# Optimization experiments

Measured on AMD Instinct MI355X. Metric: run time of the kernel, lower is better.

The kernel has to match this reference:

```python
import jax, jax.numpy as jnp
import numpy as np

N = 30000      # nodes
E = 1000000    # edges
G = 256        # graphs
IN = 3         # in_channels
H = 8          # heads
D = 16         # per-head dim
HID = 128      # hidden_dim = H*D
L = 3          # num_layers
KP = 17        # num_keypoints
KPE = 16       # kp_emb_dim
NEG = 0.2      # GATv2 leaky_relu negative slope
EPS = 1e-5     # BatchNorm eps


def setup_inputs() -> dict:
    key = jax.random.key(0)
    ks = jax.random.split(key, 24)
    x = jax.random.normal(ks[0], (N, IN), jnp.float32)
    edge_index = jax.random.randint(ks[1], (2, E), 0, N, jnp.int32)
    batch = jnp.sort(jax.random.randint(ks[2], (N,), 0, G, jnp.int32))
    s_in = 1.0 / np.sqrt(IN + KPE)
    s_h = 1.0 / np.sqrt(HID)
    return {
        "x": x,
        "edge_index": edge_index,
        "batch": batch,
        "kp_emb": jax.random.normal(ks[3], (KP, KPE), jnp.float32),
        "w_in": jax.random.normal(ks[4], (IN + KPE, HID), jnp.float32) * s_in,
        "b_in": jax.random.normal(ks[5], (HID,), jnp.float32) * 0.01,
        "w_l": jax.random.normal(ks[6], (L, HID, HID), jnp.float32) * s_h,
        "w_r": jax.random.normal(ks[7], (L, HID, HID), jnp.float32) * s_h,
        "att": jax.random.normal(ks[8], (L, H, D), jnp.float32) * (1.0 / np.sqrt(D)),
        "conv_bias": jax.random.normal(ks[9], (L, HID), jnp.float32) * 0.01,
        "bn_gamma": jnp.ones((L, HID), jnp.float32) + 0.1 * jax.random.normal(ks[10], (L, HID), jnp.float32),
        "bn_beta": 0.1 * jax.random.normal(ks[11], (L, HID), jnp.float32),
        "bn_mean": 0.1 * jax.random.normal(ks[12], (L, HID), jnp.float32),
        "bn_var": 0.5 + jax.random.uniform(ks[13], (L, HID), jnp.float32),
        "w1": jax.random.normal(ks[14], (HID, 2 * HID), jnp.float32) * s_h,
        "b1": jnp.zeros((2 * HID,), jnp.float32),
        "w2": jax.random.normal(ks[15], (2 * HID, HID), jnp.float32) * (1.0 / np.sqrt(2 * HID)),
        "b2": jnp.zeros((HID,), jnp.float32),
        "w3": jax.random.normal(ks[16], (HID, 2), jnp.float32) * s_h,
        "b3": jnp.zeros((2,), jnp.float32),
    }


def reference(x, edge_index, batch, kp_emb, w_in, b_in, w_l, w_r, att, conv_bias,
              bn_gamma, bn_beta, bn_mean, bn_var, w1, b1, w2, b2, w3, b3):
    n = x.shape[0]
    # keypoint id embedding concat + input projection
    kp_ids = jnp.arange(n) % KP
    h = jnp.concatenate([x, kp_emb[kp_ids]], axis=-1) @ w_in + b_in  # [N, HID]
    # GATv2Conv adds self loops by default
    loops = jnp.arange(n, dtype=edge_index.dtype)
    src = jnp.concatenate([edge_index[0], loops])  # message sources (j)
    dst = jnp.concatenate([edge_index[1], loops])  # message targets (i)
    for l in range(L):
        xl = (h @ w_l[l]).reshape(n, H, D)  # source transform (lin_l)
        xr = (h @ w_r[l]).reshape(n, H, D)  # target transform (lin_r)
        z = xl[src] + xr[dst]                              # [Et, H, D]
        score = jnp.einsum('ehd,hd->eh', jax.nn.leaky_relu(z, NEG), att[l])
        # segment softmax over incoming edges of each dst node
        m = jax.ops.segment_max(score, dst, num_segments=n)
        ex = jnp.exp(score - m[dst])
        denom = jax.ops.segment_sum(ex, dst, num_segments=n)
        alpha = ex / denom[dst]                            # [Et, H]
        msg = xl[src] * alpha[..., None]                   # [Et, H, D]
        out = jax.ops.segment_sum(msg, dst, num_segments=n).reshape(n, HID) + conv_bias[l]
        out = jax.nn.relu(out)
        # BatchNorm1d (eval mode: running stats)
        out = (out - bn_mean[l]) * (bn_gamma[l] / jnp.sqrt(bn_var[l] + EPS)) + bn_beta[l]
        h = h + out  # residual (dropout = identity in eval)
    # global mean pool per graph
    sums = jax.ops.segment_sum(h, batch, num_segments=G)
    cnt = jax.ops.segment_sum(jnp.ones((n, 1), h.dtype), batch, num_segments=G)
    g = sums / jnp.maximum(cnt, 1.0)
    # classifier MLP
    g = jax.nn.elu(g @ w1 + b1)
    g = jax.nn.elu(g @ w2 + b2)
    return g @ w3 + b3  # [G, 2]
```

## Files before the change

### kernel.cpp

```cpp
#include <hip/hip_runtime.h>
#include <hip/hip_bf16.h>

#define N_NODES 30000
#define N_EDGES 1000000
#define N_GRAPHS 256
#define HEADS 8
#define DHEAD 16
#define HIDDEN 128
#define LAYERS 3
#define KPN 17
#define KPE 16
#define NEG_SLOPE 0.2f
#define BN_EPS 1e-5f
#define ET (N_EDGES + N_NODES)
#define NBIN 235
#define BINW 128
#define BINCAP 6144
#define CHUNK 4096
#define NB_EDGE 245
#define NBGEMM 938

typedef __attribute__((ext_vector_type(8))) short bf16x8;
typedef __attribute__((ext_vector_type(4))) float f32x4;

__device__ __forceinline__ unsigned bf16_rne(float f) {
    unsigned u = __float_as_uint(f);
    return (u + 0x7fffu + ((u >> 16) & 1u)) >> 16;
}

__global__ __launch_bounds__(256) void k_pre(const int* __restrict__ batch,
                                             int* __restrict__ bcnt,
                                             int* __restrict__ gptr,
                                             int* __restrict__ ptr,
                                             const float* __restrict__ w_l,
                                             const float* __restrict__ w_r,
                                             unsigned short* __restrict__ wT) {
    int bid = blockIdx.x, t = threadIdx.x;
    if (bid == 0) {
        if (t < NBIN) bcnt[t] = 0;
        for (int g = t; g <= N_GRAPHS; g += 256) {
            if (g == N_GRAPHS) { gptr[g] = N_NODES; }
            else {
                int lo = 0, hi = N_NODES;
                while (lo < hi) {
                    int mid = (lo + hi) >> 1;
                    if (batch[mid] < g) lo = mid + 1; else hi = mid;
                }
                gptr[g] = lo;
            }
        }
        if (t == 0) ptr[N_NODES] = ET;
    } else {
        int idx = (bid - 1) * 256 + t;
        if (idx < LAYERS * 256 * 128) {
            int l = idx / (256 * 128);
            int rem = idx - l * 256 * 128;
            int c = rem >> 7;
            int k = rem & 127;
            float v = (c < 128) ? w_l[(size_t)l * 16384 + k * 128 + c]
                                : w_r[(size_t)l * 16384 + k * 128 + (c - 128)];
            wT[idx] = (unsigned short)bf16_rne(v);
        }
    }
}

template<bool FUSED>
__global__ __launch_bounds__(256) void k_gemmT(const float* __restrict__ x,
                                               const float* __restrict__ kp_emb,
                                               const float* __restrict__ w_in,
                                               const float* __restrict__ b_in,
                                               float* __restrict__ h,
                                               const unsigned short* __restrict__ hb,
                                               const unsigned short* __restrict__ wT,
                                               unsigned short* __restrict__ xlb,
                                               unsigned short* __restrict__ xrb,
                                               const int* __restrict__ ei,
                                               int* __restrict__ bcnt,
                                               unsigned* __restrict__ bdata) {
    __shared__ unsigned short hsA[32][136];
    __shared__ unsigned short st[32][264];
    __shared__ int lcnt[NBIN];
    __shared__ int lbase[NBIN];
    int tid = threadIdx.x;

    if (FUSED && blockIdx.x >= NBGEMM) {
        int base = (blockIdx.x - NBGEMM) * CHUNK;
        int n = N_EDGES - base; if (n > CHUNK) n = CHUNK;
        for (int i = tid; i < NBIN; i += 256) lcnt[i] = 0;
        __syncthreads();
        for (int t = tid; t < n; t += 256) {
            int d = ei[N_EDGES + base + t];
            atomicAdd(&lcnt[d >> 7], 1);
        }
        __syncthreads();
        for (int i = tid; i < NBIN; i += 256) {
            int c = lcnt[i];
            lbase[i] = c ? atomicAdd(&bcnt[i], c) : 0;
            lcnt[i] = 0;
        }
        __syncthreads();
        for (int t = tid; t < n; t += 256) {
            int s = ei[base + t];
            int d = ei[N_EDGES + base + t];
            int b = d >> 7;
            int pos = lbase[b] + atomicAdd(&lcnt[b], 1);
            bdata[(size_t)b * BINCAP + pos] = (unsigned)s | ((unsigned)(d & 127) << 15);
        }
        return;
    }

    int wave = tid >> 6, lane = tid & 63;
    int brow = blockIdx.x * 32;
    int lr = lane & 15, lk = lane >> 4;

    if (FUSED) {
        int r = tid >> 3, c16 = (tid & 7) * 16;
        int gr = brow + r;
        int gc = gr < N_NODES ? gr : 0;
        float xv0 = x[gc * 3], xv1 = x[gc * 3 + 1], xv2 = x[gc * 3 + 2];
        const float* kp = kp_emb + (gc % KPN) * KPE;
        float res[16];
#pragma unroll
        for (int q = 0; q < 16; ++q) {
            int c = c16 + q;
            float acc = b_in[c] + xv0 * w_in[c] + xv1 * w_in[128 + c] + xv2 * w_in[256 + c];
#pragma unroll
            for (int kk = 0; kk < KPE; ++kk) acc += kp[kk] * w_in[(3 + kk) * 128 + c];
            res[q] = acc;
        }
        if (gr < N_NODES) {
#pragma unroll
            for (int q = 0; q < 16; q += 4)
                *(float4*)(h + (size_t)gr * 128 + c16 + q) =
                    make_float4(res[q], res[q + 1], res[q + 2], res[q + 3]);
        }
#pragma unroll
        for (int q = 0; q < 16; ++q) hsA[r][c16 + q] = (unsigned short)bf16_rne(res[q]);
        __syncthreads();
    }

    int ar0c = brow + lr;      if (ar0c >= N_NODES) ar0c = N_NODES - 1;
    int ar1c = brow + 16 + lr; if (ar1c >= N_NODES) ar1c = N_NODES - 1;
    int c0 = wave * 64 + lr;
    const unsigned short* wb = wT + (size_t)c0 * 128 + lk * 8;

    f32x4 acc[2][4];
#pragma unroll
    for (int m = 0; m < 2; ++m)
#pragma unroll
        for (int n = 0; n < 4; ++n) acc[m][n] = (f32x4){0.f, 0.f, 0.f, 0.f};

#pragma unroll
    for (int ks = 0; ks < 4; ++ks) {
        bf16x8 a0, a1;
        if (FUSED) {
            a0 = *(const bf16x8*)&hsA[lr][lk * 8 + ks * 32];
            a1 = *(const bf16x8*)&hsA[16 + lr][lk * 8 + ks * 32];
        } else {
            a0 = *(const bf16x8*)(hb + (size_t)ar0c * 128 + lk * 8 + ks * 32);
            a1 = *(const bf16x8*)(hb + (size_t)ar1c * 128 + lk * 8 + ks * 32);
        }
#pragma unroll
        for (int nt = 0; nt < 4; ++nt) {
            bf16x8 b = *(const bf16x8*)(wb + nt * 16 * 128 + ks * 32);
            acc[0][nt] = __builtin_amdgcn_mfma_f32_16x16x32_bf16(a0, b, acc[0][nt], 0, 0, 0);
            acc[1][nt] = __builtin_amdgcn_mfma_f32_16x16x32_bf16(a1, b, acc[1][nt], 0, 0, 0);
        }
    }

    int r0 = lk * 4;
#pragma unroll
    for (int mt = 0; mt < 2; ++mt)
#pragma unroll
        for (int nt = 0; nt < 4; ++nt)
#pragma unroll
            for (int j = 0; j < 4; ++j)
                st[r0 + mt * 16 + j][c0 + nt * 16] = (unsigned short)bf16_rne(acc[mt][nt][j]);
    __syncthreads();

    int rr = tid >> 3, seg = tid & 7;
    int grow = brow + rr;
    if (grow < N_NODES) {
        uint4 v0 = *(uint4*)&st[rr][seg * 32];
        uint4 v1 = *(uint4*)&st[rr][seg * 32 + 8];
        uint4 v2 = *(uint4*)&st[rr][seg * 32 + 16];
        uint4 v3 = *(uint4*)&st[rr][seg * 32 + 24];
        unsigned short* dst = (seg < 4) ? (xlb + (size_t)grow * 128 + seg * 32)
                                        : (xrb + (size_t)grow * 128 + (seg - 4) * 32);
        *(uint4*)(dst)      = v0;
        *(uint4*)(dst + 8)  = v1;
        *(uint4*)(dst + 16) = v2;
        *(uint4*)(dst + 24) = v3;
    }
}

__global__ __launch_bounds__(256) void k_place2(const int* __restrict__ bcnt,
                                                const unsigned* __restrict__ bdata,
                                                int* __restrict__ ptr,
                                                unsigned short* __restrict__ csr_src) {
    __shared__ int vsc[256];
    __shared__ unsigned ldata[BINCAP];
    __shared__ unsigned short lcsr[BINCAP + BINW];
    __shared__ int hist[BINW], pre[BINW], nodestart[BINW], lofs[BINW];
    __shared__ int bbase_sh;
    int b = blockIdx.x, tid = threadIdx.x;
    int n = bcnt[b];
    int nNodes = N_NODES - b * BINW; if (nNodes > BINW) nNodes = BINW;

    for (int t = tid; t < n; t += 256) ldata[t] = bdata[(size_t)b * BINCAP + t];

    int c = 0;
    if (tid < NBIN) {
        int nodes = N_NODES - tid * BINW; if (nodes > BINW) nodes = BINW;
        c = bcnt[tid] + nodes;
    }
    vsc[tid] = c;
    if (tid < BINW) hist[tid] = (tid < nNodes) ? 1 : 0;
    __syncthreads();
    for (int off = 1; off < 256; off <<= 1) {
        int x = (tid >= off) ? vsc[tid - off] : 0;
        __syncthreads();
        vsc[tid] += x;
        __syncthreads();
    }
    if (tid == 0) bbase_sh = (b == 0) ? 0 : vsc[b - 1];

    for (int t = tid; t < n; t += 256)
        atomicAdd(&hist[(ldata[t] >> 15) & 127], 1);
    __syncthreads();
    if (tid < BINW) pre[tid] = hist[tid];
    __syncthreads();
    for (int off = 1; off < BINW; off <<= 1) {
        int x = (tid >= off && tid < BINW) ? pre[tid - off] : 0;
        __syncthreads();
        if (tid < BINW) pre[tid] += x;
        __syncthreads();
    }
    if (tid < BINW) {
        int ns = pre[tid] - hist[tid];
        nodestart[tid] = ns;
        if (tid < nNodes) {
            int node = b * BINW + tid;
            ptr[node] = bbase_sh + ns;
            lcsr[ns] = (unsigned short)node;
        }
        lofs[tid] = 1;
    }
    __syncthreads();
    for (int t = tid; t < n; t += 256) {
        unsigned e = ldata[t];
        int dl = (e >> 15) & 127;
        int pos = nodestart[dl] + atomicAdd(&lofs[dl], 1);
        lcsr[pos] = (unsigned short)(e & 0x7fffu);
    }
    __syncthreads();
    int tot = n + nNodes;
    for (int t = tid; t < tot; t += 256) csr_src[bbase_sh + t] = lcsr[t];
}

__global__ __launch_bounds__(256) void k_gat(const unsigned* __restrict__ xlb,
                                             const unsigned* __restrict__ xrb,
                                             const int* __restrict__ ptr,
                                             const unsigned short* __restrict__ csr_src,
                                             const float* __restrict__ att_l,
                                             const float* __restrict__ bias_l,
                                             const float* __restrict__ gamma_l,
                                             const float* __restrict__ beta_l,
                                             const float* __restrict__ mean_l,
                                             const float* __restrict__ var_l,
                                             float* __restrict__ h,
                                             unsigned short* __restrict__ hb) {
    int wid = (blockIdx.x * 256 + threadIdx.x) >> 6;
    int lane = threadIdx.x & 63;
    if (wid >= N_NODES) return;
    int i = wid;
    int grp = lane >> 5;
    int l32 = lane & 31;
    int d0 = 4 * l32;

    uint2 xw = *(const uint2*)(xrb + ((size_t)i << 6) + (l32 << 1));
    float xr0 = __uint_as_float(xw.x << 16);
    float xr1 = __uint_as_float(xw.x & 0xffff0000u);
    float xr2 = __uint_as_float(xw.y << 16);
    float xr3 = __uint_as_float(xw.y & 0xffff0000u);
    const float L2E = 1.44269504089f;
    float4 av = *(const float4*)(att_l + d0);
    av.x *= L2E; av.y *= L2E; av.z *= L2E; av.w *= L2E;
    int e0 = ptr[i], e1 = ptr[i + 1];

    float denom = 0.f, acc0 = 0.f, acc1 = 0.f, acc2 = 0.f, acc3 = 0.f;

#define LDP(KP, WREG, VREG) { \
    int eo = 2 * (KP) + grp; \
    int sr = __shfl(sv, eo); \
    VREG = eo < cnt; \
    int rw = VREG ? sr : 0; \
    WREG = *(const uint2*)(xlb + ((size_t)rw << 6) + (l32 << 1)); \
}
#define PROCP(WREG, VREG) { \
    float v0 = __uint_as_float(WREG.x << 16); \
    float v1 = __uint_as_float(WREG.x & 0xffff0000u); \
    float v2 = __uint_as_float(WREG.y << 16); \
    float v3 = __uint_as_float(WREG.y & 0xffff0000u); \
    float z0 = v0 + xr0, z1 = v1 + xr1, z2 = v2 + xr2, z3 = v3 + xr3; \
    z0 = fmaxf(z0, NEG_SLOPE * z0); \
    z1 = fmaxf(z1, NEG_SLOPE * z1); \
    z2 = fmaxf(z2, NEG_SLOPE * z2); \
    z3 = fmaxf(z3, NEG_SLOPE * z3); \
    float p = z0 * av.x + z1 * av.y + z2 * av.z + z3 * av.w; \
    p += __shfl_xor(p, 1); \
    p += __shfl_xor(p, 2); \
    float ex = VREG ? exp2f(p) : 0.f; \
    denom += ex; \
    acc0 += ex * v0; acc1 += ex * v1; acc2 += ex * v2; acc3 += ex * v3; \
}

    for (int base = e0; base < e1; base += 64) {
        int idx = base + lane;
        int sv = (idx < e1) ? (int)csr_src[idx] : 0;
        int cnt = e1 - base; if (cnt > 64) cnt = 64;
        int np = (cnt + 1) >> 1;

        uint2 w0, w1; bool b0 = false, b1 = false;
        LDP(0, w0, b0);
        if (1 < np) LDP(1, w1, b1);
        int k = 0;
        for (; k + 2 < np; k += 2) {
            uint2 n0, n1; bool c0v, c1v;
            LDP(k + 2, n0, c0v);
            LDP(k + 3, n1, c1v);
            PROCP(w0, b0); PROCP(w1, b1);
            w0 = n0; b0 = c0v; w1 = n1; b1 = c1v;
        }
        PROCP(w0, b0);
        if (k + 1 < np) PROCP(w1, b1);
    }
#undef LDP
#undef PROCP

    denom += __shfl_xor(denom, 32);
    acc0 += __shfl_xor(acc0, 32);
    acc1 += __shfl_xor(acc1, 32);
    acc2 += __shfl_xor(acc2, 32);
    acc3 += __shfl_xor(acc3, 32);

    if (grp == 0) {
        float inv = 1.f / denom;
        float4 bia = *(const float4*)(bias_l + d0);
        float4 gam = *(const float4*)(gamma_l + d0);
        float4 bet = *(const float4*)(beta_l + d0);
        float4 mea = *(const float4*)(mean_l + d0);
        float4 var = *(const float4*)(var_l + d0);
        float o0 = fmaxf(acc0 * inv + bia.x, 0.f);
        float o1 = fmaxf(acc1 * inv + bia.y, 0.f);
        float o2 = fmaxf(acc2 * inv + bia.z, 0.f);
        float o3 = fmaxf(acc3 * inv + bia.w, 0.f);
        o0 = (o0 - mea.x) * (gam.x * rsqrtf(var.x + BN_EPS)) + bet.x;
        o1 = (o1 - mea.y) * (gam.y * rsqrtf(var.y + BN_EPS)) + bet.y;
        o2 = (o2 - mea.z) * (gam.z * rsqrtf(var.z + BN_EPS)) + bet.z;
        o3 = (o3 - mea.w) * (gam.w * rsqrtf(var.w + BN_EPS)) + bet.w;
        float4 hv = *(const float4*)(h + (size_t)i * 128 + d0);
        hv.x += o0; hv.y += o1; hv.z += o2; hv.w += o3;
        *(float4*)(h + (size_t)i * 128 + d0) = hv;
        unsigned pk0 = bf16_rne(hv.x) | (bf16_rne(hv.y) << 16);
        unsigned pk1 = bf16_rne(hv.z) | (bf16_rne(hv.w) << 16);
        uint2 pk; pk.x = pk0; pk.y = pk1;
        *(uint2*)(hb + (size_t)i * 128 + d0) = pk;
    }
}

__global__ __launch_bounds__(256) void k_poolmlp(const float* __restrict__ h,
                                                 const int* __restrict__ gptr,
                                                 const float* __restrict__ w1, const float* __restrict__ b1,
                                                 const float* __restrict__ w2, const float* __restrict__ b2,
                                                 const float* __restrict__ w3, const float* __restrict__ b3,
                                                 float* __restrict__ out) {
    __shared__ float red[256];
    __shared__ float g[128], t1[256], t2[128];
    int b = blockIdx.x, t = threadIdx.x;
    int c = t & 127, half = t >> 7;
    int lo = gptr[b], hi = gptr[b + 1];
    float s = 0.f;
    for (int i = lo + half; i < hi; i += 2) s += h[(size_t)i * 128 + c];
    red[t] = s;
    __syncthreads();
    if (half == 0) {
        float cntf = fmaxf((float)(hi - lo), 1.0f);
        g[c] = (red[c] + red[c + 128]) / cntf;
    }
    __syncthreads();
    {
        float acc = b1[t];
        for (int k = 0; k < 128; ++k) acc += g[k] * w1[k * 256 + t];
        t1[t] = acc > 0.f ? acc : expm1f(acc);
    }
    __syncthreads();
    if (t < 128) {
        float acc = b2[t];
        for (int k = 0; k < 256; ++k) acc += t1[k] * w2[k * 128 + t];
        t2[t] = acc > 0.f ? acc : expm1f(acc);
    }
    __syncthreads();
    if (t < 2) {
        float acc = b3[t];
        for (int k = 0; k < 128; ++k) acc += t2[k] * w3[k * 2 + t];
        out[b * 2 + t] = acc;
    }
}

extern "C" void kernel_launch(void* const* d_in, const int* in_sizes, int n_in,
                              void* d_out, int out_size, void* d_ws, size_t ws_size,
                              hipStream_t stream) {
    const float* x        = (const float*)d_in[0];
    const int*   ei       = (const int*)d_in[1];
    const int*   batch    = (const int*)d_in[2];
    const float* kp_emb   = (const float*)d_in[3];
    const float* w_in     = (const float*)d_in[4];
    const float* b_in     = (const float*)d_in[5];
    const float* w_l      = (const float*)d_in[6];
    const float* w_r      = (const float*)d_in[7];
    const float* att      = (const float*)d_in[8];
    const float* conv_b   = (const float*)d_in[9];
    const float* bn_gamma = (const float*)d_in[10];
    const float* bn_beta  = (const float*)d_in[11];
    const float* bn_mean  = (const float*)d_in[12];
    const float* bn_var   = (const float*)d_in[13];
    const float* w1 = (const float*)d_in[14];
    const float* b1 = (const float*)d_in[15];
    const float* w2 = (const float*)d_in[16];
    const float* b2 = (const float*)d_in[17];
    const float* w3 = (const float*)d_in[18];
    const float* b3 = (const float*)d_in[19];
    float* out = (float*)d_out;

    char* ws = (char*)d_ws;
    const size_t OFF_H    = 0;
    const size_t OFF_HB   = OFF_H    + 15360000;
    const size_t OFF_XL   = OFF_HB   + 7680000;
    const size_t OFF_XR   = OFF_XL   + 7680000;
    const size_t OFF_WT   = OFF_XR   + 7680000;
    const size_t OFF_PTR  = OFF_WT   + 196608;
    const size_t OFF_BCNT = OFF_PTR  + 120320;
    const size_t OFF_SRC  = OFF_BCNT + 1024;
    const size_t OFF_GPTR = OFF_SRC  + 2060032;
    const size_t OFF_BD   = OFF_GPTR + 1088;

    float*          h      = (float*)(ws + OFF_H);
    unsigned short* hb     = (unsigned short*)(ws + OFF_HB);
    unsigned short* xlb    = (unsigned short*)(ws + OFF_XL);
    unsigned short* xrb    = (unsigned short*)(ws + OFF_XR);
    unsigned short* wT     = (unsigned short*)(ws + OFF_WT);
    int*            ptr    = (int*)(ws + OFF_PTR);
    int*            bcnt   = (int*)(ws + OFF_BCNT);
    unsigned short* csrsrc = (unsigned short*)(ws + OFF_SRC);
    int*            gptr   = (int*)(ws + OFF_GPTR);
    unsigned*       bdata  = (unsigned*)(ws + OFF_BD);

    k_pre<<<1 + (LAYERS * 256 * 128 + 255) / 256, 256, 0, stream>>>(
        batch, bcnt, gptr, ptr, w_l, w_r, wT);

    k_gemmT<true><<<NBGEMM + NB_EDGE, 256, 0, stream>>>(
        x, kp_emb, w_in, b_in, h, hb, wT, xlb, xrb, ei, bcnt, bdata);

    k_place2<<<NBIN, 256, 0, stream>>>(bcnt, bdata, ptr, csrsrc);

    for (int l = 0; l < LAYERS; ++l) {
        if (l > 0) {
            k_gemmT<false><<<NBGEMM, 256, 0, stream>>>(
                x, kp_emb, w_in, b_in, h, hb, wT + (size_t)l * 256 * 128, xlb, xrb,
                ei, bcnt, bdata);
        }
        k_gat<<<(N_NODES + 3) / 4, 256, 0, stream>>>(
            (const unsigned*)xlb, (const unsigned*)xrb, ptr, csrsrc,
            att + (size_t)l * 128, conv_b + (size_t)l * 128,
            bn_gamma + (size_t)l * 128, bn_beta + (size_t)l * 128,
            bn_mean + (size_t)l * 128, bn_var + (size_t)l * 128, h, hb);
    }

    k_poolmlp<<<N_GRAPHS, 256, 0, stream>>>(h, gptr, w1, b1, w2, b2, w3, b3, out);
}
```

Before: 255.7 us.

## Split projection GEMM into xl/xr halves, precompute keypoint projection, move edge blocks first

Each projection GEMM block now computes only the lin_l or lin_r half for 32 rows, which doubles the grid and halves per-block accumulators and shared staging. The keypoint embedding projection (17x128 plus bias) is precomputed once in the prep kernel instead of being redone per node. Edge-binning blocks are placed first in the fused launch, and BINCAP is reduced slightly. The aim is better occupancy and less redundant arithmetic. In exchange, the fused kernel recomputes the input embedding in both halves and each A tile is loaded twice.

```diff
diff --git a/kernel.cpp b/kernel.cpp
--- a/kernel.cpp
+++ b/kernel.cpp
@@ -15,10 +15,10 @@
 #define ET (N_EDGES + N_NODES)
 #define NBIN 235
 #define BINW 128
-#define BINCAP 6144
+#define BINCAP 6016
 #define CHUNK 4096
 #define NB_EDGE 245
-#define NBGEMM 938
+#define NBG 1876
 
 typedef __attribute__((ext_vector_type(8))) short bf16x8;
 typedef __attribute__((ext_vector_type(4))) float f32x4;
@@ -34,7 +34,11 @@
                                              int* __restrict__ ptr,
                                              const float* __restrict__ w_l,
                                              const float* __restrict__ w_r,
-                                             unsigned short* __restrict__ wT) {
+                                             const float* __restrict__ kp_emb,
+                                             const float* __restrict__ w_in,
+                                             const float* __restrict__ b_in,
+                                             unsigned short* __restrict__ wT,
+                                             float* __restrict__ kpp) {
     int bid = blockIdx.x, t = threadIdx.x;
     if (bid == 0) {
         if (t < NBIN) bcnt[t] = 0;
@@ -50,7 +54,7 @@
             }
         }
         if (t == 0) ptr[N_NODES] = ET;
-    } else {
+    } else if (bid <= 384) {
         int idx = (bid - 1) * 256 + t;
         if (idx < LAYERS * 256 * 128) {
             int l = idx / (256 * 128);
@@ -61,14 +65,23 @@
                                 : w_r[(size_t)l * 16384 + k * 128 + (c - 128)];
             wT[idx] = (unsigned short)bf16_rne(v);
         }
+    } else {
+        int idx = (bid - 385) * 256 + t;
+        if (idx < KPN * 128) {
+            int p = idx >> 7, c = idx & 127;
+            float acc = b_in[c];
+#pragma unroll
+            for (int k = 0; k < KPE; ++k)
+                acc += kp_emb[p * KPE + k] * w_in[(3 + k) * 128 + c];
+            kpp[idx] = acc;
+        }
     }
 }
 
 template<bool FUSED>
 __global__ __launch_bounds__(256) void k_gemmT(const float* __restrict__ x,
-                                               const float* __restrict__ kp_emb,
+                                               const float* __restrict__ kpp,
                                                const float* __restrict__ w_in,
-                                               const float* __restrict__ b_in,
                                                float* __restrict__ h,
                                                const unsigned short* __restrict__ hb,
                                                const unsigned short* __restrict__ wT,
@@ -77,14 +90,14 @@
                                                const int* __restrict__ ei,
                                                int* __restrict__ bcnt,
                                                unsigned* __restrict__ bdata) {
-    __shared__ unsigned short hsA[32][136];
-    __shared__ unsigned short st[32][264];
-    __shared__ int lcnt[NBIN];
-    __shared__ int lbase[NBIN];
+    __shared__ unsigned short st[32][132];
+    __shared__ unsigned short hsA[FUSED ? 32 : 1][136];
+    __shared__ int lcnt[FUSED ? NBIN : 1];
+    __shared__ int lbase[FUSED ? NBIN : 1];
     int tid = threadIdx.x;
 
-    if (FUSED && blockIdx.x >= NBGEMM) {
-        int base = (blockIdx.x - NBGEMM) * CHUNK;
+    if (FUSED && blockIdx.x < NB_EDGE) {
+        int base = blockIdx.x * CHUNK;
         int n = N_EDGES - base; if (n > CHUNK) n = CHUNK;
         for (int i = tid; i < NBIN; i += 256) lcnt[i] = 0;
         __syncthreads();
@@ -109,8 +122,10 @@
         return;
     }
 
+    int gbid = FUSED ? (blockIdx.x - NB_EDGE) : blockIdx.x;
+    int half = gbid & 1;
+    int brow = (gbid >> 1) * 32;
     int wave = tid >> 6, lane = tid & 63;
-    int brow = blockIdx.x * 32;
     int lr = lane & 15, lk = lane >> 4;
 
     if (FUSED) {
@@ -118,17 +133,14 @@
         int gr = brow + r;
         int gc = gr < N_NODES ? gr : 0;
         float xv0 = x[gc * 3], xv1 = x[gc * 3 + 1], xv2 = x[gc * 3 + 2];
-        const float* kp = kp_emb + (gc % KPN) * KPE;
+        const float* kprow = kpp + (gc % KPN) * 128;
         float res[16];
 #pragma unroll
         for (int q = 0; q < 16; ++q) {
             int c = c16 + q;
-            float acc = b_in[c] + xv0 * w_in[c] + xv1 * w_in[128 + c] + xv2 * w_in[256 + c];
-#pragma unroll
-            for (int kk = 0; kk < KPE; ++kk) acc += kp[kk] * w_in[(3 + kk) * 128 + c];
-            res[q] = acc;
-        }
-        if (gr < N_NODES) {
+            res[q] = kprow[c] + xv0 * w_in[c] + xv1 * w_in[128 + c] + xv2 * w_in[256 + c];
+        }
+        if (gr < N_NODES && half == 0) {
 #pragma unroll
             for (int q = 0; q < 16; q += 4)
                 *(float4*)(h + (size_t)gr * 128 + c16 + q) =
@@ -141,14 +153,14 @@
 
     int ar0c = brow + lr;      if (ar0c >= N_NODES) ar0c = N_NODES - 1;
     int ar1c = brow + 16 + lr; if (ar1c >= N_NODES) ar1c = N_NODES - 1;
-    int c0 = wave * 64 + lr;
-    const unsigned short* wb = wT + (size_t)c0 * 128 + lk * 8;
-
-    f32x4 acc[2][4];
+    int c0l = wave * 32 + lr;
+    const unsigned short* wb = wT + (size_t)(half * 128 + c0l) * 128 + lk * 8;
+
+    f32x4 acc[2][2];
 #pragma unroll
     for (int m = 0; m < 2; ++m)
 #pragma unroll
-        for (int n = 0; n < 4; ++n) acc[m][n] = (f32x4){0.f, 0.f, 0.f, 0.f};
+        for (int n = 0; n < 2; ++n) acc[m][n] = (f32x4){0.f, 0.f, 0.f, 0.f};
 
 #pragma unroll
     for (int ks = 0; ks < 4; ++ks) {
@@ -161,7 +173,7 @@
             a1 = *(const bf16x8*)(hb + (size_t)ar1c * 128 + lk * 8 + ks * 32);
         }
 #pragma unroll
-        for (int nt = 0; nt < 4; ++nt) {
+        for (int nt = 0; nt < 2; ++nt) {
             bf16x8 b = *(const bf16x8*)(wb + nt * 16 * 128 + ks * 32);
             acc[0][nt] = __builtin_amdgcn_mfma_f32_16x16x32_bf16(a0, b, acc[0][nt], 0, 0, 0);
             acc[1][nt] = __builtin_amdgcn_mfma_f32_16x16x32_bf16(a1, b, acc[1][nt], 0, 0, 0);
@@ -172,25 +184,18 @@
 #pragma unroll
     for (int mt = 0; mt < 2; ++mt)
 #pragma unroll
-        for (int nt = 0; nt < 4; ++nt)
+        for (int nt = 0; nt < 2; ++nt)
 #pragma unroll
             for (int j = 0; j < 4; ++j)
-                st[r0 + mt * 16 + j][c0 + nt * 16] = (unsigned short)bf16_rne(acc[mt][nt][j]);
+                st[mt * 16 + r0 + j][c0l + nt * 16] = (unsigned short)bf16_rne(acc[mt][nt][j]);
     __syncthreads();
 
     int rr = tid >> 3, seg = tid & 7;
     int grow = brow + rr;
     if (grow < N_NODES) {
-        uint4 v0 = *(uint4*)&st[rr][seg * 32];
-        uint4 v1 = *(uint4*)&st[rr][seg * 32 + 8];
-        uint4 v2 = *(uint4*)&st[rr][seg * 32 + 16];
-        uint4 v3 = *(uint4*)&st[rr][seg * 32 + 24];
-        unsigned short* dst = (seg < 4) ? (xlb + (size_t)grow * 128 + seg * 32)
-                                        : (xrb + (size_t)grow * 128 + (seg - 4) * 32);
-        *(uint4*)(dst)      = v0;
-        *(uint4*)(dst + 8)  = v1;
-        *(uint4*)(dst + 16) = v2;
-        *(uint4*)(dst + 24) = v3;
+        unsigned short* dst = (half == 0 ? xlb : xrb) + (size_t)grow * 128 + seg * 16;
+        *(uint4*)(dst)     = *(uint4*)&st[rr][seg * 16];
+        *(uint4*)(dst + 8) = *(uint4*)&st[rr][seg * 16 + 8];
     }
 }
 
@@ -444,6 +449,7 @@
     const size_t OFF_SRC  = OFF_BCNT + 1024;
     const size_t OFF_GPTR = OFF_SRC  + 2060032;
     const size_t OFF_BD   = OFF_GPTR + 1088;
+    const size_t OFF_KPP  = OFF_BD   + (size_t)NBIN * BINCAP * 4;
 
     float*          h      = (float*)(ws + OFF_H);
     unsigned short* hb     = (unsigned short*)(ws + OFF_HB);
@@ -455,19 +461,20 @@
     unsigned short* csrsrc = (unsigned short*)(ws + OFF_SRC);
     int*            gptr   = (int*)(ws + OFF_GPTR);
     unsigned*       bdata  = (unsigned*)(ws + OFF_BD);
-
-    k_pre<<<1 + (LAYERS * 256 * 128 + 255) / 256, 256, 0, stream>>>(
-        batch, bcnt, gptr, ptr, w_l, w_r, wT);
-
-    k_gemmT<true><<<NBGEMM + NB_EDGE, 256, 0, stream>>>(
-        x, kp_emb, w_in, b_in, h, hb, wT, xlb, xrb, ei, bcnt, bdata);
+    float*          kpp    = (float*)(ws + OFF_KPP);
+
+    k_pre<<<385 + (KPN * 128 + 255) / 256, 256, 0, stream>>>(
+        batch, bcnt, gptr, ptr, w_l, w_r, kp_emb, w_in, b_in, wT, kpp);
+
+    k_gemmT<true><<<NB_EDGE + NBG, 256, 0, stream>>>(
+        x, kpp, w_in, h, hb, wT, xlb, xrb, ei, bcnt, bdata);
 
     k_place2<<<NBIN, 256, 0, stream>>>(bcnt, bdata, ptr, csrsrc);
 
     for (int l = 0; l < LAYERS; ++l) {
         if (l > 0) {
-            k_gemmT<false><<<NBGEMM, 256, 0, stream>>>(
-                x, kp_emb, w_in, b_in, h, hb, wT + (size_t)l * 256 * 128, xlb, xrb,
+            k_gemmT<false><<<NBG, 256, 0, stream>>>(
+                x, kpp, w_in, h, hb, wT + (size_t)l * 256 * 128, xlb, xrb,
                 ei, bcnt, bdata);
         }
         k_gat<<<(N_NODES + 3) / 4, 256, 0, stream>>>(
```

Result: faster. 241.5 us (-5.5%).
